# Optimization experiments

Measured on AMD Instinct MI355X. Metric: run time of the kernel, lower is better.

Reference implementation:

```python
import jax, jax.numpy as jnp
import numpy as np


def setup_inputs() -> dict:
    key = jax.random.key(0)
    k1, k2 = jax.random.split(key)
    B, H, W = 64, 1024, 1024
    output = jax.random.normal(k1, (B, H, W), dtype=jnp.float32)
    target = jax.random.normal(k2, (B, H, W), dtype=jnp.float32)
    return {"output": output, "target": target, "patch_size": 64}


def reference(output, target, patch_size):
    # output, target: [B, H, W]; tile into non-overlapping p x p patches,
    # per-patch mean |o - t|, max over patches per image, mean over batch.
    B, H, W = output.shape
    p = patch_size
    nh, nw = H // p, W // p
    diff = jnp.abs(output - target)                      # [B, H, W]
    # [B, nh, p, nw, p] -> per-patch mean over the two p axes
    patch_l1 = diff.reshape(B, nh, p, nw, p).mean(axis=(2, 4))  # [B, nh, nw]
    max_patch_loss = patch_l1.max(axis=(1, 2))           # [B]
    # original initializes max at 0; L1 >= 0 so max with 0 is a no-op, kept for fidelity
    max_patch_loss = jnp.maximum(max_patch_loss, 0.0)
    return max_patch_loss.mean()
```

## Files before the change

### kernel.cpp

```cpp
#include <hip/hip_runtime.h>

#define BATCH   64
#define HEIGHT  1024
#define WIDTH   1024
#define PSZ     64
#define NPH     16
#define NPW     16

__global__ __launch_bounds__(256) void patch_rowstrip_kernel(
    const float* __restrict__ out_p, const float* __restrict__ tgt_p,
    float* __restrict__ blk_max)
{
    const int blk  = blockIdx.x;
    const int img  = blk >> 4;
    const int prow = blk & 15;

    const size_t base = (size_t)img * (HEIGHT * (size_t)WIDTH)
                      + (size_t)prow * PSZ * WIDTH
                      + (size_t)threadIdx.x * 4;

    const float4* __restrict__ po = reinterpret_cast<const float4*>(out_p + base);
    const float4* __restrict__ pt = reinterpret_cast<const float4*>(tgt_p + base);
    const int row_stride_f4 = WIDTH / 4;

    float s0 = 0.f, s1 = 0.f;
#pragma unroll 8
    for (int r = 0; r < PSZ; ++r) {
        const float4 a = po[(size_t)r * row_stride_f4];
        const float4 c = pt[(size_t)r * row_stride_f4];
        s0 += fabsf(a.x - c.x) + fabsf(a.y - c.y);
        s1 += fabsf(a.z - c.z) + fabsf(a.w - c.w);
    }
    float s = s0 + s1;

#pragma unroll
    for (int off = 8; off > 0; off >>= 1)
        s += __shfl_down(s, off, 16);

    __shared__ float lds[NPW];
    if ((threadIdx.x & 15) == 0) lds[threadIdx.x >> 4] = s;
    __syncthreads();
    if (threadIdx.x == 0) {
        float m = lds[0];
#pragma unroll
        for (int i = 1; i < NPW; ++i) m = fmaxf(m, lds[i]);
        blk_max[blk] = m * (1.0f / (PSZ * PSZ));
    }
}

__global__ __launch_bounds__(256) void final_reduce_kernel(
    const float* __restrict__ blk_max, float* __restrict__ result)
{
    const int t = threadIdx.x;
    const float4 v = reinterpret_cast<const float4*>(blk_max)[t];
    float m = fmaxf(fmaxf(v.x, v.y), fmaxf(v.z, v.w));
    m = fmaxf(m, __shfl_down(m, 2, 4));
    m = fmaxf(m, __shfl_down(m, 1, 4));
    float contrib = ((t & 3) == 0) ? m : 0.0f;
#pragma unroll
    for (int off = 32; off > 0; off >>= 1)
        contrib += __shfl_down(contrib, off, 64);

    __shared__ float lds[4];
    if ((t & 63) == 0) lds[t >> 6] = contrib;
    __syncthreads();
    if (t == 0)
        result[0] = (lds[0] + lds[1] + lds[2] + lds[3]) * (1.0f / BATCH);
}

extern "C" void kernel_launch(void* const* d_in, const int* in_sizes, int n_in,
                              void* d_out, int out_size, void* d_ws, size_t ws_size,
                              hipStream_t stream) {
    const float* out_p = (const float*)d_in[0];
    const float* tgt_p = (const float*)d_in[1];
    float* blk_max = (float*)d_ws;
    float* result  = (float*)d_out;

    patch_rowstrip_kernel<<<BATCH * NPH, 256, 0, stream>>>(out_p, tgt_p, blk_max);
    final_reduce_kernel<<<1, 256, 0, stream>>>(blk_max, result);
}
```

Before: 500.9 us.

## Split patch strips into half-strips and add a per-image max reduction kernel

The main kernel now gives each block half of a 64-row patch strip, which doubles the grid to 2048 blocks and unrolls loads four rows at a time for more memory-level parallelism. Per-patch partial sums are written to workspace without a block-level LDS max. A new per-image kernel combines the halves and takes the max, and a third kernel takes the mean. The aim is higher occupancy and better bandwidth use, at the cost of an extra kernel launch and more intermediate traffic.

Measured after the change: 503.6 us. No clear change (+0.5%).

```diff
diff --git a/kernel.cpp b/kernel.cpp
--- a/kernel.cpp
+++ b/kernel.cpp
@@ -6,66 +6,78 @@
 #define PSZ     64
 #define NPH     16
 #define NPW     16
+#define HALFROWS 32
 
-__global__ __launch_bounds__(256) void patch_rowstrip_kernel(
+#define ABS4(a,b) (fabsf((a).x-(b).x)+fabsf((a).y-(b).y)+fabsf((a).z-(b).z)+fabsf((a).w-(b).w))
+
+__global__ __launch_bounds__(256) void patch_halfstrip_kernel(
     const float* __restrict__ out_p, const float* __restrict__ tgt_p,
-    float* __restrict__ blk_max)
+    float* __restrict__ part)
 {
     const int blk  = blockIdx.x;
-    const int img  = blk >> 4;
-    const int prow = blk & 15;
+    const int img  = blk >> 5;
+    const int prow = (blk >> 1) & 15;
+    const int half = blk & 1;
 
-    const size_t base = (size_t)img * (HEIGHT * (size_t)WIDTH)
-                      + (size_t)prow * PSZ * WIDTH
-                      + (size_t)threadIdx.x * 4;
+    const size_t base_f4 = (size_t)img * (HEIGHT * WIDTH / 4)
+                         + (size_t)(prow * PSZ + half * HALFROWS) * (WIDTH / 4)
+                         + threadIdx.x;
+    const float4* __restrict__ po = reinterpret_cast<const float4*>(out_p) + base_f4;
+    const float4* __restrict__ pt = reinterpret_cast<const float4*>(tgt_p) + base_f4;
 
-    const float4* __restrict__ po = reinterpret_cast<const float4*>(out_p + base);
-    const float4* __restrict__ pt = reinterpret_cast<const float4*>(tgt_p + base);
-    const int row_stride_f4 = WIDTH / 4;
-
-    float s0 = 0.f, s1 = 0.f;
-#pragma unroll 8
-    for (int r = 0; r < PSZ; ++r) {
-        const float4 a = po[(size_t)r * row_stride_f4];
-        const float4 c = pt[(size_t)r * row_stride_f4];
-        s0 += fabsf(a.x - c.x) + fabsf(a.y - c.y);
-        s1 += fabsf(a.z - c.z) + fabsf(a.w - c.w);
+    float s0 = 0.f, s1 = 0.f, s2 = 0.f, s3 = 0.f;
+#pragma unroll
+    for (int r = 0; r < HALFROWS; r += 4) {
+        const float4 a0 = po[(size_t)(r + 0) * 256];
+        const float4 a1 = po[(size_t)(r + 1) * 256];
+        const float4 a2 = po[(size_t)(r + 2) * 256];
+        const float4 a3 = po[(size_t)(r + 3) * 256];
+        const float4 b0 = pt[(size_t)(r + 0) * 256];
+        const float4 b1 = pt[(size_t)(r + 1) * 256];
+        const float4 b2 = pt[(size_t)(r + 2) * 256];
+        const float4 b3 = pt[(size_t)(r + 3) * 256];
+        s0 += ABS4(a0, b0);
+        s1 += ABS4(a1, b1);
+        s2 += ABS4(a2, b2);
+        s3 += ABS4(a3, b3);
     }
-    float s = s0 + s1;
+    float s = (s0 + s1) + (s2 + s3);
 
 #pragma unroll
     for (int off = 8; off > 0; off >>= 1)
         s += __shfl_down(s, off, 16);
 
-    __shared__ float lds[NPW];
-    if ((threadIdx.x & 15) == 0) lds[threadIdx.x >> 4] = s;
-    __syncthreads();
-    if (threadIdx.x == 0) {
-        float m = lds[0];
-#pragma unroll
-        for (int i = 1; i < NPW; ++i) m = fmaxf(m, lds[i]);
-        blk_max[blk] = m * (1.0f / (PSZ * PSZ));
-    }
+    if ((threadIdx.x & 15) == 0)
+        part[blk * NPW + (threadIdx.x >> 4)] = s;
 }
 
-__global__ __launch_bounds__(256) void final_reduce_kernel(
-    const float* __restrict__ blk_max, float* __restrict__ result)
+__global__ __launch_bounds__(256) void image_max_kernel(
+    const float* __restrict__ part, float* __restrict__ img_max)
 {
-    const int t = threadIdx.x;
-    const float4 v = reinterpret_cast<const float4*>(blk_max)[t];
-    float m = fmaxf(fmaxf(v.x, v.y), fmaxf(v.z, v.w));
-    m = fmaxf(m, __shfl_down(m, 2, 4));
-    m = fmaxf(m, __shfl_down(m, 1, 4));
-    float contrib = ((t & 3) == 0) ? m : 0.0f;
+    const int img = blockIdx.x;
+    const int t   = threadIdx.x;
+    const int idx = img * 512 + (t >> 4) * 32 + (t & 15);
+    float ps = (part[idx] + part[idx + 16]) * (1.0f / (PSZ * PSZ));
+
 #pragma unroll
     for (int off = 32; off > 0; off >>= 1)
-        contrib += __shfl_down(contrib, off, 64);
+        ps = fmaxf(ps, __shfl_down(ps, off, 64));
 
     __shared__ float lds[4];
-    if ((t & 63) == 0) lds[t >> 6] = contrib;
+    if ((t & 63) == 0) lds[t >> 6] = ps;
     __syncthreads();
     if (t == 0)
-        result[0] = (lds[0] + lds[1] + lds[2] + lds[3]) * (1.0f / BATCH);
+        img_max[img] = fmaxf(fmaxf(lds[0], lds[1]), fmaxf(lds[2], lds[3]));
+}
+
+__global__ __launch_bounds__(64) void mean_kernel(
+    const float* __restrict__ img_max, float* __restrict__ result)
+{
+    float v = img_max[threadIdx.x];
+#pragma unroll
+    for (int off = 32; off > 0; off >>= 1)
+        v += __shfl_down(v, off, 64);
+    if (threadIdx.x == 0) result[0] = v * (1.0f / BATCH);
 }
 
 extern "C" void kernel_launch(void* const* d_in, const int* in_sizes, int n_in,
@@ -73,9 +85,11 @@
                               hipStream_t stream) {
     const float* out_p = (const float*)d_in[0];
     const float* tgt_p = (const float*)d_in[1];
-    float* blk_max = (float*)d_ws;
+    float* part    = (float*)d_ws;
+    float* img_max = part + BATCH * NPH * 2 * NPW;
     float* result  = (float*)d_out;
 
-    patch_rowstrip_kernel<<<BATCH * NPH, 256, 0, stream>>>(out_p, tgt_p, blk_max);
-    final_reduce_kernel<<<1, 256, 0, stream>>>(blk_max, result);
+    patch_halfstrip_kernel<<<BATCH * NPH * 2, 256, 0, stream>>>(out_p, tgt_p, part);
+    image_max_kernel<<<BATCH, 256, 0, stream>>>(part, img_max);
+    mean_kernel<<<1, 64, 0, stream>>>(img_max, result);
 }
```
